# Performance work log

Measured on AMD Instinct MI355X. Metric: run time of the kernel, lower is better.

## Reference

```python
import jax, jax.numpy as jnp
import numpy as np

B, H, W, C = 64, 56, 56, 96
NH, WS, SS = 3, 7, 3
HID = 4 * C
N = WS * WS              # tokens per window = 49
NW = (H // WS) * (W // WS)  # windows per image = 64
HD = C // NH             # head dim = 32
SCALE = HD ** -0.5


def _rel_pos_index():
    coords = np.stack(np.meshgrid(np.arange(WS), np.arange(WS), indexing='ij'))  # (2, WS, WS)
    cf = coords.reshape(2, -1)                      # (2, N)
    rel = cf[:, :, None] - cf[:, None, :]           # (2, N, N)
    rel = rel.transpose(1, 2, 0)                    # (N, N, 2)
    rel[:, :, 0] += WS - 1
    rel[:, :, 1] += WS - 1
    rel[:, :, 0] *= 2 * WS - 1
    return rel.sum(-1)                              # (N, N) int


def _attn_mask():
    # shift-window mask per original Swin: label regions, mask cross-region pairs with -100
    img = np.zeros((H, W))
    cnt = 0
    sl = (slice(0, -WS), slice(-WS, -SS), slice(-SS, None))
    for hs in sl:
        for ws_ in sl:
            img[hs, ws_] = cnt
            cnt += 1
    mw = img.reshape(H // WS, WS, W // WS, WS).transpose(0, 2, 1, 3).reshape(-1, N)  # (NW, N)
    am = mw[:, None, :] - mw[:, :, None]
    return np.where(am != 0, -100.0, 0.0).astype(np.float32)  # (NW, N, N)


REL_IDX = jnp.asarray(_rel_pos_index())
ATTN_MASK = jnp.asarray(_attn_mask())


def _ln(x, g, b):
    m = x.mean(-1, keepdims=True)
    v = x.var(-1, keepdims=True)
    return (x - m) / jnp.sqrt(v + 1e-5) * g + b


def setup_inputs() -> dict:
    key = jax.random.key(0)
    ks = jax.random.split(key, 8)
    s = lambda k, shape: jax.random.normal(k, shape, jnp.float32) * 0.02
    return dict(
        x=jax.random.normal(ks[0], (B, H * W, C), jnp.float32),
        norm1_g=jnp.ones((C,), jnp.float32), norm1_b=jnp.zeros((C,), jnp.float32),
        qkv_w=s(ks[1], (3 * C, C)), qkv_b=jnp.zeros((3 * C,), jnp.float32),
        rpb_table=s(ks[2], ((2 * WS - 1) ** 2, NH)),
        proj_w=s(ks[3], (C, C)), proj_b=jnp.zeros((C,), jnp.float32),
        norm2_g=jnp.ones((C,), jnp.float32), norm2_b=jnp.zeros((C,), jnp.float32),
        fc1_w=s(ks[4], (HID, C)), fc1_b=jnp.zeros((HID,), jnp.float32),
        fc2_w=s(ks[5], (C, HID)), fc2_b=jnp.zeros((C,), jnp.float32),
    )


def reference(x, norm1_g, norm1_b, qkv_w, qkv_b, rpb_table, proj_w, proj_b,
              norm2_g, norm2_b, fc1_w, fc1_b, fc2_w, fc2_b):
    shortcut = x                                    # (B, H*W, C)
    h = _ln(x, norm1_g, norm1_b).reshape(B, H, W, C)
    # cyclic shift for SW-MSA
    h = jnp.roll(h, (-SS, -SS), axis=(1, 2))
    # window partition -> (B*NW, N, C)
    hw = h.reshape(B, H // WS, WS, W // WS, WS, C).transpose(0, 1, 3, 2, 4, 5).reshape(B * NW, N, C)
    # qkv projection
    qkv = (hw @ qkv_w.T + qkv_b).reshape(B * NW, N, 3, NH, HD).transpose(2, 0, 3, 1, 4)
    q, k, v = qkv[0] * SCALE, qkv[1], qkv[2]        # each (B*NW, NH, N, HD)
    attn = jnp.einsum('bhnd,bhmd->bhnm', q, k)      # (B*NW, NH, N, N)
    # relative position bias gather: (N, N, NH) -> (NH, N, N)
    bias = rpb_table[REL_IDX].transpose(2, 0, 1)
    attn = attn + bias[None]
    # shift mask: broadcast over batch and heads
    attn = attn.reshape(B, NW, NH, N, N) + ATTN_MASK[None, :, None]
    attn = jax.nn.softmax(attn.reshape(B * NW, NH, N, N), axis=-1)
    out = jnp.einsum('bhnm,bhmd->bhnd', attn, v).transpose(0, 2, 1, 3).reshape(B * NW, N, C)
    out = out @ proj_w.T + proj_b
    # window reverse + reverse shift
    out = out.reshape(B, H // WS, W // WS, WS, WS, C).transpose(0, 1, 3, 2, 4, 5).reshape(B, H, W, C)
    out = jnp.roll(out, (SS, SS), axis=(1, 2)).reshape(B, H * W, C)
    x = shortcut + out
    # MLP with residual (erf-based GELU, matching torch nn.GELU default)
    h2 = _ln(x, norm2_g, norm2_b)
    h2 = jax.nn.gelu(h2 @ fc1_w.T + fc1_b, approximate=False) @ fc2_w.T + fc2_b
    return x + h2
```

## Files before the change

### kernel.cpp

```cpp
#include <hip/hip_runtime.h>
#include <math.h>

#define BB   64
#define HH   56
#define WWD  56
#define CCH  96
#define SSS  3
#define NTK  49
#define TOKENS (BB*HH*WWD)

typedef unsigned short ushort;
typedef short short8 __attribute__((ext_vector_type(8)));
typedef float floatx4 __attribute__((ext_vector_type(4)));

__device__ __forceinline__ ushort f2bf(float f) {
    __bf16 h = (__bf16)f;
    ushort u; __builtin_memcpy(&u, &h, 2); return u;
}

__device__ __forceinline__ float fast_gelu(float v) {
    float u = v * (1.5957691216f + 0.071354816f * (v * v));
    float r = __builtin_amdgcn_rcpf(__expf(u) + 1.f);
    return v - v * r;
}

#define WQKV  0
#define WPROJ (54*512)
#define WFC1  (72*512)
#define WFC2  (144*512)
#define NFRAG 216

__global__ __launch_bounds__(256) void wconv(
    const float* __restrict__ qkv_w, const float* __restrict__ proj_w,
    const float* __restrict__ fc1_w, const float* __restrict__ fc2_w,
    ushort* __restrict__ wsb)
{
    int tg = blockIdx.x * 256 + threadIdx.x;
    int frag = tg >> 6, lane = tg & 63, l15 = lane & 15, quad = lane >> 4;
    const float* src; int row, kbase, K;
    if (frag < 54)       { int f = frag;       int ct = f/3,  kt = f%3;  src = qkv_w;  row = ct*16+l15; kbase = kt*32+quad*8; K = 96;  }
    else if (frag < 72)  { int f = frag - 54;  int ct = f/3,  kt = f%3;  src = proj_w; row = ct*16+l15; kbase = kt*32+quad*8; K = 96;  }
    else if (frag < 144) { int f = frag - 72;  int ct = f/3,  kt = f%3;  src = fc1_w;  row = ct*16+l15; kbase = kt*32+quad*8; K = 96;  }
    else                 { int f = frag - 144; int ct = f/12, hc = f%12; src = fc2_w;  row = ct*16+l15; kbase = hc*32+quad*8; K = 384; }
    const float* p = src + (size_t)row * K + kbase;
    ushort tmp[8];
    #pragma unroll
    for (int j = 0; j < 8; ++j) tmp[j] = f2bf(p[j]);
    *(short8*)(wsb + (size_t)frag * 512 + lane * 8) = *(const short8*)tmp;
}

__global__ __launch_bounds__(256, 4) void swin_kernel(
    const float* __restrict__ x,
    const float* __restrict__ n1g, const float* __restrict__ n1b,
    const ushort* __restrict__ wsb,
    const float* __restrict__ qkv_b, const float* __restrict__ rpb,
    const float* __restrict__ proj_b,
    const float* __restrict__ n2g, const float* __restrict__ n2b,
    const float* __restrict__ fc1_b, const float* __restrict__ fc2_b,
    float* __restrict__ out)
{
    __shared__ ushort xa[64][100];
    __shared__ float  kvf[6464];
    __shared__ float2 rpb2[169];
    __shared__ float  rpb1[169];

    ushort (*ks)[100] = (ushort(*)[100])kvf;
    ushort (*vt)[68]  = (ushort(*)[68])((ushort*)kvf + 64*100);

    const int wgid = blockIdx.x;
    const int b  = wgid >> 6;
    const int wy = (wgid >> 3) & 7;
    const int wx = wgid & 7;
    const int tid  = threadIdx.x;
    const int lane = tid & 63;
    const int wv   = tid >> 6;
    const int l15  = lane & 15;
    const int quad = lane >> 4;
    const int m0   = wv * 16;

    for (int i = tid; i < 169; i += 256) {
        float2 t; t.x = rpb[3*i]; t.y = rpb[3*i+1];
        rpb2[i] = t;
        rpb1[i] = rpb[3*i+2];
    }

    int rowm[4], rowy[4], rowx[4], rowli[4], gofs[4];
    #pragma unroll
    for (int r = 0; r < 4; ++r) {
        int m = m0 + quad * 4 + r;
        rowm[r] = m;
        int yi = m / 7, xi = m - 7 * yi;
        rowy[r] = yi; rowx[r] = xi;
        int ri = wy * 7 + yi, ci = wx * 7 + xi;
        rowli[r] = (ri < 49 ? 0 : (ri < 53 ? 1 : 2)) * 3 + (ci < 49 ? 0 : (ci < 53 ? 1 : 2));
        int rr = ri + SSS; if (rr >= HH)  rr -= HH;
        int cc = ci + SSS; if (cc >= WWD) cc -= WWD;
        gofs[r] = ((b * HH + rr) * WWD + cc) * CCH;
    }

    {
        float gn1[6], bn1[6];
        #pragma unroll
        for (int ct = 0; ct < 6; ++ct) { gn1[ct] = n1g[ct*16+l15]; bn1[ct] = n1b[ct*16+l15]; }
        #pragma unroll
        for (int r = 0; r < 4; ++r) {
            float xv[6];
            if (rowm[r] < NTK) {
                #pragma unroll
                for (int ct = 0; ct < 6; ++ct) xv[ct] = x[gofs[r] + ct*16 + l15];
            } else {
                #pragma unroll
                for (int ct = 0; ct < 6; ++ct) xv[ct] = 0.f;
            }
            float s = 0.f, q = 0.f;
            #pragma unroll
            for (int ct = 0; ct < 6; ++ct) { s += xv[ct]; q += xv[ct] * xv[ct]; }
            #pragma unroll
            for (int o = 1; o < 16; o <<= 1) { s += __shfl_xor(s, o); q += __shfl_xor(q, o); }
            float mean = s * (1.f / 96.f);
            float rstd = rsqrtf(q * (1.f / 96.f) - mean * mean + 1e-5f);
            #pragma unroll
            for (int ct = 0; ct < 6; ++ct)
                xa[rowm[r]][ct*16 + l15] = f2bf((xv[ct] - mean) * rstd * gn1[ct] + bn1[ct]);
        }
    }

    short8 axh[3];
    #pragma unroll
    for (int kt = 0; kt < 3; ++kt) axh[kt] = *(const short8*)&xa[m0 + l15][kt * 32 + quad * 8];

    float qreg[6][4];
    {
        short8 bwp[3];
        #pragma unroll
        for (int kt = 0; kt < 3; ++kt)
            bwp[kt] = *(const short8*)(wsb + WQKV + (size_t)kt * 512 + lane * 8);
        for (int ct = 0; ct < 18; ++ct) {
            short8 b0 = bwp[0], b1 = bwp[1], b2 = bwp[2];
            if (ct < 17) {
                #pragma unroll
                for (int kt = 0; kt < 3; ++kt)
                    bwp[kt] = *(const short8*)(wsb + WQKV + (size_t)((ct + 1) * 3 + kt) * 512 + lane * 8);
            }
            floatx4 acc = {0.f, 0.f, 0.f, 0.f};
            acc = __builtin_amdgcn_mfma_f32_16x16x32_bf16(axh[0], b0, acc, 0, 0, 0);
            acc = __builtin_amdgcn_mfma_f32_16x16x32_bf16(axh[1], b1, acc, 0, 0, 0);
            acc = __builtin_amdgcn_mfma_f32_16x16x32_bf16(axh[2], b2, acc, 0, 0, 0);
            int oc = ct * 16 + l15;
            float bias = qkv_b[oc];
            if (ct < 6) {
                #pragma unroll
                for (int r = 0; r < 4; ++r) qreg[ct][r] = (acc[r] + bias) * 0.17677669529663687f;
            } else if (ct < 12) {
                #pragma unroll
                for (int r = 0; r < 4; ++r) ks[m0 + quad * 4 + r][oc - 96] = f2bf(acc[r] + bias);
            } else {
                unsigned u0 = (unsigned)f2bf(acc[0] + bias) | ((unsigned)f2bf(acc[1] + bias) << 16);
                unsigned u1 = (unsigned)f2bf(acc[2] + bias) | ((unsigned)f2bf(acc[3] + bias) << 16);
                uint2 pk2; pk2.x = u0; pk2.y = u1;
                *(uint2*)&vt[oc - 192][m0 + quad * 4] = pk2;
            }
        }
    }
    #pragma unroll
    for (int ct = 0; ct < 6; ++ct)
        #pragma unroll
        for (int r = 0; r < 4; ++r)
            xa[m0 + quad * 4 + r][ct * 16 + l15] = f2bf(qreg[ct][r]);
    short8 aq[3];
    #pragma unroll
    for (int h = 0; h < 3; ++h) aq[h] = *(const short8*)&xa[m0 + l15][h * 32 + quad * 8];
    __syncthreads();

    int ql = m0 + l15;
    int qy = ql / 7, qx = ql - 7 * qy;
    int rq = wy * 7 + qy, cq = wx * 7 + qx;
    int lq = (rq < 49 ? 0 : (rq < 53 ? 1 : 2)) * 3 + (cq < 49 ? 0 : (cq < 53 ? 1 : 2));
    int qok = ql < NTK;
    int rixT[4][4]; float baddT[4][4];
    #pragma unroll
    for (int ct = 0; ct < 4; ++ct) {
        #pragma unroll
        for (int r = 0; r < 4; ++r) {
            int k = ct * 16 + quad * 4 + r;
            int ky = k / 7, kx = k - 7 * ky;
            int rk = wy * 7 + ky, ck = wx * 7 + kx;
            int lk = (rk < 49 ? 0 : (rk < 53 ? 1 : 2)) * 3 + (ck < 49 ? 0 : (ck < 53 ? 1 : 2));
            int ok = qok && (k < NTK);
            rixT[ct][r] = ok ? ((qy - ky + 6) * 13 + (qx - kx + 6)) : 0;
            baddT[ct][r] = !ok ? -1e30f : (lq != lk ? -100.f : 0.f);
        }
    }

    const int s0 = ((quad & 1) << 5) + l15;
    const int s1 = s0 + 16;
    const bool hisel = quad >= 2;

    float by1[4][4];
    #pragma unroll
    for (int h = 0; h < 3; ++h) {
        const int hb = 32 * h;
        float st[4][4];
        #pragma unroll
        for (int ct = 0; ct < 4; ++ct) {
            short8 ak = *(const short8*)&ks[ct * 16 + l15][hb + quad * 8];
            floatx4 acc = {0.f, 0.f, 0.f, 0.f};
            acc = __builtin_amdgcn_mfma_f32_16x16x32_bf16(ak, aq[h], acc, 0, 0, 0);
            #pragma unroll
            for (int r = 0; r < 4; ++r) {
                float bias;
                if (h == 0)      { float2 bb = rpb2[rixT[ct][r]]; bias = bb.x; by1[ct][r] = bb.y; }
                else if (h == 1) { bias = by1[ct][r]; }
                else             { bias = rpb1[rixT[ct][r]]; }
                st[ct][r] = __expf(acc[r] + bias + baddT[ct][r]);
            }
        }
        float u0 = (st[0][0] + st[0][1]) + (st[0][2] + st[0][3]);
        float u1 = (st[1][0] + st[1][1]) + (st[1][2] + st[1][3]);
        float u2 = (st[2][0] + st[2][1]) + (st[2][2] + st[2][3]);
        float u3 = (st[3][0] + st[3][1]) + (st[3][2] + st[3][3]);
        float sum = (u0 + u1) + (u2 + u3);
        sum += __shfl_xor(sum, 16);
        sum += __shfl_xor(sum, 32);
        float inv = __builtin_amdgcn_rcpf(sum);
        unsigned pk[4][2];
        #pragma unroll
        for (int ct = 0; ct < 4; ++ct) {
            pk[ct][0] = (unsigned)f2bf(st[ct][0] * inv) | ((unsigned)f2bf(st[ct][1] * inv) << 16);
            pk[ct][1] = (unsigned)f2bf(st[ct][2] * inv) | ((unsigned)f2bf(st[ct][3] * inv) << 16);
        }
        unsigned p00a = __shfl(pk[0][0], s0), p01a = __shfl(pk[0][1], s0);
        unsigned p00b = __shfl(pk[0][0], s1), p01b = __shfl(pk[0][1], s1);
        unsigned p10a = __shfl(pk[1][0], s0), p11a = __shfl(pk[1][1], s0);
        unsigned p10b = __shfl(pk[1][0], s1), p11b = __shfl(pk[1][1], s1);
        unsigned p20a = __shfl(pk[2][0], s0), p21a = __shfl(pk[2][1], s0);
        unsigned p20b = __shfl(pk[2][0], s1), p21b = __shfl(pk[2][1], s1);
        unsigned p30a = __shfl(pk[3][0], s0), p31a = __shfl(pk[3][1], s0);
        unsigned p30b = __shfl(pk[3][0], s1), p31b = __shfl(pk[3][1], s1);
        union { unsigned u[4]; short8 v; } a0, a1;
        a0.u[0] = hisel ? p10a : p00a;
        a0.u[1] = hisel ? p11a : p01a;
        a0.u[2] = hisel ? p10b : p00b;
        a0.u[3] = hisel ? p11b : p01b;
        a1.u[0] = hisel ? p30a : p20a;
        a1.u[1] = hisel ? p31a : p21a;
        a1.u[2] = hisel ? p30b : p20b;
        a1.u[3] = hisel ? p31b : p21b;
        #pragma unroll
        for (int nt = 0; nt < 2; ++nt) {
            floatx4 acc = {0.f, 0.f, 0.f, 0.f};
            short8 bv0 = *(const short8*)&vt[hb + nt * 16 + l15][quad * 8];
            short8 bv1 = *(const short8*)&vt[hb + nt * 16 + l15][32 + quad * 8];
            acc = __builtin_amdgcn_mfma_f32_16x16x32_bf16(a0.v, bv0, acc, 0, 0, 0);
            acc = __builtin_amdgcn_mfma_f32_16x16x32_bf16(a1.v, bv1, acc, 0, 0, 0);
            #pragma unroll
            for (int r = 0; r < 4; ++r)
                xa[rowm[r]][hb + nt * 16 + l15] = f2bf(acc[r]);
        }
    }

    __syncthreads();

    short8 axp[3];
    #pragma unroll
    for (int kt = 0; kt < 3; ++kt) axp[kt] = *(const short8*)&xa[m0 + l15][kt * 32 + quad * 8];
    float xrv[6][4];
    {
        short8 bwp[3];
        #pragma unroll
        for (int kt = 0; kt < 3; ++kt)
            bwp[kt] = *(const short8*)(wsb + WPROJ + (size_t)kt * 512 + lane * 8);
        for (int ct = 0; ct < 6; ++ct) {
            short8 b0 = bwp[0], b1 = bwp[1], b2 = bwp[2];
            if (ct < 5) {
                #pragma unroll
                for (int kt = 0; kt < 3; ++kt)
                    bwp[kt] = *(const short8*)(wsb + WPROJ + (size_t)((ct + 1) * 3 + kt) * 512 + lane * 8);
            }
            floatx4 acc = {0.f, 0.f, 0.f, 0.f};
            acc = __builtin_amdgcn_mfma_f32_16x16x32_bf16(axp[0], b0, acc, 0, 0, 0);
            acc = __builtin_amdgcn_mfma_f32_16x16x32_bf16(axp[1], b1, acc, 0, 0, 0);
            acc = __builtin_amdgcn_mfma_f32_16x16x32_bf16(axp[2], b2, acc, 0, 0, 0);
            int c2 = ct * 16 + l15;
            float pb = proj_b[c2];
            #pragma unroll
            for (int r = 0; r < 4; ++r) {
                float v = 0.f;
                if (rowm[r] < NTK) v = acc[r] + pb + x[gofs[r] + c2];
                xrv[ct][r] = v;
            }
        }
    }

    float gn[6], bn[6];
    #pragma unroll
    for (int ct = 0; ct < 6; ++ct) { gn[ct] = n2g[ct * 16 + l15]; bn[ct] = n2b[ct * 16 + l15]; }
    #pragma unroll
    for (int r = 0; r < 4; ++r) {
        float s = 0.f, q = 0.f;
        #pragma unroll
        for (int ct = 0; ct < 6; ++ct) { s += xrv[ct][r]; q += xrv[ct][r] * xrv[ct][r]; }
        #pragma unroll
        for (int o = 1; o < 16; o <<= 1) { s += __shfl_xor(s, o); q += __shfl_xor(q, o); }
        float mean = s * (1.f / 96.f);
        float rstd = rsqrtf(q * (1.f / 96.f) - mean * mean + 1e-5f);
        #pragma unroll
        for (int ct = 0; ct < 6; ++ct)
            xa[rowm[r]][ct * 16 + l15] =
                f2bf((xrv[ct][r] - mean) * rstd * gn[ct] + bn[ct]);
    }

    short8 axn[3];
    #pragma unroll
    for (int kt = 0; kt < 3; ++kt) axn[kt] = *(const short8*)&xa[m0 + l15][kt * 32 + quad * 8];
    ushort* actb = (ushort*)kvf + wv * 1280;
    floatx4 o2[6];
    #pragma unroll
    for (int ct = 0; ct < 6; ++ct) o2[ct] = (floatx4){0.f, 0.f, 0.f, 0.f};

    short8 aprev;
    for (int hc = 0; hc < 12; ++hc) {
        floatx4 a1c[2];
        #pragma unroll
        for (int c2t = 0; c2t < 2; ++c2t) {
            floatx4 acc = {0.f, 0.f, 0.f, 0.f};
            #pragma unroll
            for (int kt = 0; kt < 3; ++kt) {
                short8 bw = *(const short8*)(wsb + WFC1 + (size_t)((hc * 2 + c2t) * 3 + kt) * 512 + lane * 8);
                acc = __builtin_amdgcn_mfma_f32_16x16x32_bf16(axn[kt], bw, acc, 0, 0, 0);
            }
            a1c[c2t] = acc;
        }
        if (hc > 0)
            aprev = *(const short8*)(actb + ((hc - 1) & 1) * 640 + l15 * 40 + quad * 8);
        #pragma unroll
        for (int c2t = 0; c2t < 2; ++c2t) {
            float b1 = fc1_b[(hc * 2 + c2t) * 16 + l15];
            #pragma unroll
            for (int r = 0; r < 4; ++r) {
                float g = fast_gelu(a1c[c2t][r] + b1);
                actb[(hc & 1) * 640 + (quad * 4 + r) * 40 + c2t * 16 + l15] = f2bf(g);
            }
        }
        if (hc > 0) {
            #pragma unroll
            for (int ct = 0; ct < 6; ++ct) {
                short8 bw = *(const short8*)(wsb + WFC2 + (size_t)(ct * 12 + hc - 1) * 512 + lane * 8);
                o2[ct] = __builtin_amdgcn_mfma_f32_16x16x32_bf16(aprev, bw, o2[ct], 0, 0, 0);
            }
        }
    }
    aprev = *(const short8*)(actb + 640 + l15 * 40 + quad * 8);
    #pragma unroll
    for (int ct = 0; ct < 6; ++ct) {
        short8 bw = *(const short8*)(wsb + WFC2 + (size_t)(ct * 12 + 11) * 512 + lane * 8);
        o2[ct] = __builtin_amdgcn_mfma_f32_16x16x32_bf16(aprev, bw, o2[ct], 0, 0, 0);
    }

    for (int ct = 0; ct < 6; ++ct) {
        int c = ct * 16 + l15;
        float b2 = fc2_b[c];
        #pragma unroll
        for (int r = 0; r < 4; ++r) {
            if (rowm[r] >= NTK) continue;
            out[gofs[r] + c] = xrv[ct][r] + o2[ct][r] + b2;
        }
    }
}

extern "C" void kernel_launch(void* const* d_in, const int* in_sizes, int n_in,
                              void* d_out, int out_size, void* d_ws, size_t ws_size,
                              hipStream_t stream) {
    const float* x      = (const float*)d_in[0];
    const float* n1g    = (const float*)d_in[1];
    const float* n1b    = (const float*)d_in[2];
    const float* qkv_w  = (const float*)d_in[3];
    const float* qkv_b  = (const float*)d_in[4];
    const float* rpb    = (const float*)d_in[5];
    const float* proj_w = (const float*)d_in[6];
    const float* proj_b = (const float*)d_in[7];
    const float* n2g    = (const float*)d_in[8];
    const float* n2b    = (const float*)d_in[9];
    const float* fc1_w  = (const float*)d_in[10];
    const float* fc1_b  = (const float*)d_in[11];
    const float* fc2_w  = (const float*)d_in[12];
    const float* fc2_b  = (const float*)d_in[13];
    float* out = (float*)d_out;
    ushort* wsb = (ushort*)d_ws;

    wconv<<<NFRAG / 4, 256, 0, stream>>>(qkv_w, proj_w, fc1_w, fc2_w, wsb);
    swin_kernel<<<BB * 64, 256, 0, stream>>>(
        x, n1g, n1b, wsb, qkv_b, rpb, proj_b, n2g, n2b, fc1_b, fc2_b, out);
}
```

Baseline: 359.4 us.

## Alias K tile with activation buffer to cut LDS and raise occupancy

Merges the separate activation buffer and K buffer into one shared array. The Q, K and V projections are split into three sequential loops so Q can be pulled into registers before K overwrites the same rows. A barrier is added inside the per-head attention loop so attention outputs never overwrite K columns still being read by other waves. Launch bounds rise from 4 to 5 blocks per CU to use the smaller LDS footprint, at the cost of extra per-head barriers and a tighter per-thread register budget that could cause spills.

```diff
diff --git a/kernel.cpp b/kernel.cpp
--- a/kernel.cpp
+++ b/kernel.cpp
@@ -49,7 +49,7 @@
     *(short8*)(wsb + (size_t)frag * 512 + lane * 8) = *(const short8*)tmp;
 }
 
-__global__ __launch_bounds__(256, 4) void swin_kernel(
+__global__ __launch_bounds__(256, 5) void swin_kernel(
     const float* __restrict__ x,
     const float* __restrict__ n1g, const float* __restrict__ n1b,
     const ushort* __restrict__ wsb,
@@ -59,13 +59,12 @@
     const float* __restrict__ fc1_b, const float* __restrict__ fc2_b,
     float* __restrict__ out)
 {
-    __shared__ ushort xa[64][100];
-    __shared__ float  kvf[6464];
+    __shared__ ushort sh[12928];
     __shared__ float2 rpb2[169];
     __shared__ float  rpb1[169];
 
-    ushort (*ks)[100] = (ushort(*)[100])kvf;
-    ushort (*vt)[68]  = (ushort(*)[68])((ushort*)kvf + 64*100);
+    ushort (*xs)[100] = (ushort(*)[100])sh;
+    ushort (*vt)[68]  = (ushort(*)[68])(sh + 6400);
 
     const int wgid = blockIdx.x;
     const int b  = wgid >> 6;
@@ -121,13 +120,13 @@
             float rstd = rsqrtf(q * (1.f / 96.f) - mean * mean + 1e-5f);
             #pragma unroll
             for (int ct = 0; ct < 6; ++ct)
-                xa[rowm[r]][ct*16 + l15] = f2bf((xv[ct] - mean) * rstd * gn1[ct] + bn1[ct]);
+                xs[rowm[r]][ct*16 + l15] = f2bf((xv[ct] - mean) * rstd * gn1[ct] + bn1[ct]);
         }
     }
 
     short8 axh[3];
     #pragma unroll
-    for (int kt = 0; kt < 3; ++kt) axh[kt] = *(const short8*)&xa[m0 + l15][kt * 32 + quad * 8];
+    for (int kt = 0; kt < 3; ++kt) axh[kt] = *(const short8*)&xs[m0 + l15][kt * 32 + quad * 8];
 
     float qreg[6][4];
     {
@@ -135,41 +134,77 @@
         #pragma unroll
         for (int kt = 0; kt < 3; ++kt)
             bwp[kt] = *(const short8*)(wsb + WQKV + (size_t)kt * 512 + lane * 8);
-        for (int ct = 0; ct < 18; ++ct) {
+        for (int ct = 0; ct < 6; ++ct) {
             short8 b0 = bwp[0], b1 = bwp[1], b2 = bwp[2];
-            if (ct < 17) {
+            if (ct < 5) {
                 #pragma unroll
                 for (int kt = 0; kt < 3; ++kt)
                     bwp[kt] = *(const short8*)(wsb + WQKV + (size_t)((ct + 1) * 3 + kt) * 512 + lane * 8);
+            }
+            floatx4 acc = {0.f, 0.f, 0.f, 0.f};
+            acc = __builtin_amdgcn_mfma_f32_16x16x32_bf16(axh[0], b0, acc, 0, 0, 0);
+            acc = __builtin_amdgcn_mfma_f32_16x16x32_bf16(axh[1], b1, acc, 0, 0, 0);
+            acc = __builtin_amdgcn_mfma_f32_16x16x32_bf16(axh[2], b2, acc, 0, 0, 0);
+            float bias = qkv_b[ct * 16 + l15];
+            #pragma unroll
+            for (int r = 0; r < 4; ++r) qreg[ct][r] = (acc[r] + bias) * 0.17677669529663687f;
+        }
+    }
+    #pragma unroll
+    for (int ct = 0; ct < 6; ++ct)
+        #pragma unroll
+        for (int r = 0; r < 4; ++r)
+            xs[m0 + quad * 4 + r][ct * 16 + l15] = f2bf(qreg[ct][r]);
+    short8 aq[3];
+    #pragma unroll
+    for (int h = 0; h < 3; ++h) aq[h] = *(const short8*)&xs[m0 + l15][h * 32 + quad * 8];
+
+    {
+        short8 bwp[3];
+        #pragma unroll
+        for (int kt = 0; kt < 3; ++kt)
+            bwp[kt] = *(const short8*)(wsb + WQKV + (size_t)(6 * 3 + kt) * 512 + lane * 8);
+        for (int ct = 0; ct < 6; ++ct) {
+            short8 b0 = bwp[0], b1 = bwp[1], b2 = bwp[2];
+            if (ct < 5) {
+                #pragma unroll
+                for (int kt = 0; kt < 3; ++kt)
+                    bwp[kt] = *(const short8*)(wsb + WQKV + (size_t)((ct + 7) * 3 + kt) * 512 + lane * 8);
             }
             floatx4 acc = {0.f, 0.f, 0.f, 0.f};
             acc = __builtin_amdgcn_mfma_f32_16x16x32_bf16(axh[0], b0, acc, 0, 0, 0);
             acc = __builtin_amdgcn_mfma_f32_16x16x32_bf16(axh[1], b1, acc, 0, 0, 0);
             acc = __builtin_amdgcn_mfma_f32_16x16x32_bf16(axh[2], b2, acc, 0, 0, 0);
             int oc = ct * 16 + l15;
-            float bias = qkv_b[oc];
-            if (ct < 6) {
-                #pragma unroll
-                for (int r = 0; r < 4; ++r) qreg[ct][r] = (acc[r] + bias) * 0.17677669529663687f;
-            } else if (ct < 12) {
-                #pragma unroll
-                for (int r = 0; r < 4; ++r) ks[m0 + quad * 4 + r][oc - 96] = f2bf(acc[r] + bias);
-            } else {
-                unsigned u0 = (unsigned)f2bf(acc[0] + bias) | ((unsigned)f2bf(acc[1] + bias) << 16);
-                unsigned u1 = (unsigned)f2bf(acc[2] + bias) | ((unsigned)f2bf(acc[3] + bias) << 16);
-                uint2 pk2; pk2.x = u0; pk2.y = u1;
-                *(uint2*)&vt[oc - 192][m0 + quad * 4] = pk2;
-            }
-        }
-    }
-    #pragma unroll
-    for (int ct = 0; ct < 6; ++ct)
-        #pragma unroll
-        for (int r = 0; r < 4; ++r)
-            xa[m0 + quad * 4 + r][ct * 16 + l15] = f2bf(qreg[ct][r]);
-    short8 aq[3];
-    #pragma unroll
-    for (int h = 0; h < 3; ++h) aq[h] = *(const short8*)&xa[m0 + l15][h * 32 + quad * 8];
+            float bias = qkv_b[96 + oc];
+            #pragma unroll
+            for (int r = 0; r < 4; ++r) xs[m0 + quad * 4 + r][oc] = f2bf(acc[r] + bias);
+        }
+    }
+    {
+        short8 bwp[3];
+        #pragma unroll
+        for (int kt = 0; kt < 3; ++kt)
+            bwp[kt] = *(const short8*)(wsb + WQKV + (size_t)(12 * 3 + kt) * 512 + lane * 8);
+        for (int ct = 0; ct < 6; ++ct) {
+            short8 b0 = bwp[0], b1 = bwp[1], b2 = bwp[2];
+            if (ct < 5) {
+                #pragma unroll
+                for (int kt = 0; kt < 3; ++kt)
+                    bwp[kt] = *(const short8*)(wsb + WQKV + (size_t)((ct + 13) * 3 + kt) * 512 + lane * 8);
+            }
+            floatx4 acc = {0.f, 0.f, 0.f, 0.f};
+            acc = __builtin_amdgcn_mfma_f32_16x16x32_bf16(axh[0], b0, acc, 0, 0, 0);
+            acc = __builtin_amdgcn_mfma_f32_16x16x32_bf16(axh[1], b1, acc, 0, 0, 0);
+            acc = __builtin_amdgcn_mfma_f32_16x16x32_bf16(axh[2], b2, acc, 0, 0, 0);
+            int oc = ct * 16 + l15;
+            float bias = qkv_b[192 + oc];
+            unsigned u0 = (unsigned)f2bf(acc[0] + bias) | ((unsigned)f2bf(acc[1] + bias) << 16);
+            unsigned u1 = (unsigned)f2bf(acc[2] + bias) | ((unsigned)f2bf(acc[3] + bias) << 16);
+            uint2 pk2; pk2.x = u0; pk2.y = u1;
+            *(uint2*)&vt[oc][m0 + quad * 4] = pk2;
+        }
+    }
     __syncthreads();
 
     int ql = m0 + l15;
@@ -203,7 +238,7 @@
         float st[4][4];
         #pragma unroll
         for (int ct = 0; ct < 4; ++ct) {
-            short8 ak = *(const short8*)&ks[ct * 16 + l15][hb + quad * 8];
+            short8 ak = *(const short8*)&xs[ct * 16 + l15][hb + quad * 8];
             floatx4 acc = {0.f, 0.f, 0.f, 0.f};
             acc = __builtin_amdgcn_mfma_f32_16x16x32_bf16(ak, aq[h], acc, 0, 0, 0);
             #pragma unroll
@@ -215,6 +250,7 @@
                 st[ct][r] = __expf(acc[r] + bias + baddT[ct][r]);
             }
         }
+        __syncthreads();
         float u0 = (st[0][0] + st[0][1]) + (st[0][2] + st[0][3]);
         float u1 = (st[1][0] + st[1][1]) + (st[1][2] + st[1][3]);
         float u2 = (st[2][0] + st[2][1]) + (st[2][2] + st[2][3]);
@@ -255,7 +291,7 @@
             acc = __builtin_amdgcn_mfma_f32_16x16x32_bf16(a1.v, bv1, acc, 0, 0, 0);
             #pragma unroll
             for (int r = 0; r < 4; ++r)
-                xa[rowm[r]][hb + nt * 16 + l15] = f2bf(acc[r]);
+                xs[rowm[r]][hb + nt * 16 + l15] = f2bf(acc[r]);
         }
     }
 
@@ -263,7 +299,7 @@
 
     short8 axp[3];
     #pragma unroll
-    for (int kt = 0; kt < 3; ++kt) axp[kt] = *(const short8*)&xa[m0 + l15][kt * 32 + quad * 8];
+    for (int kt = 0; kt < 3; ++kt) axp[kt] = *(const short8*)&xs[m0 + l15][kt * 32 + quad * 8];
     float xrv[6][4];
     {
         short8 bwp[3];
@@ -306,14 +342,14 @@
         float rstd = rsqrtf(q * (1.f / 96.f) - mean * mean + 1e-5f);
         #pragma unroll
         for (int ct = 0; ct < 6; ++ct)
-            xa[rowm[r]][ct * 16 + l15] =
+            xs[rowm[r]][ct * 16 + l15] =
                 f2bf((xrv[ct][r] - mean) * rstd * gn[ct] + bn[ct]);
     }
 
     short8 axn[3];
     #pragma unroll
-    for (int kt = 0; kt < 3; ++kt) axn[kt] = *(const short8*)&xa[m0 + l15][kt * 32 + quad * 8];
-    ushort* actb = (ushort*)kvf + wv * 1280;
+    for (int kt = 0; kt < 3; ++kt) axn[kt] = *(const short8*)&xs[m0 + l15][kt * 32 + quad * 8];
+    ushort* actb = sh + 6400 + wv * 1280;
     floatx4 o2[6];
     #pragma unroll
     for (int ct = 0; ct < 6; ++ct) o2[ct] = (floatx4){0.f, 0.f, 0.f, 0.f};
```

After: 452.4 us. 1.26x slower.
